# Kernel tuning notes

Hardware: AMD Instinct MI355X
Metric: run time of the kernel (lower is better)

## Reference

```python
import jax, jax.numpy as jnp
import numpy as np

NC = 80          # num classes (len(yolov8.names))
CONF = 0.25      # ultralytics conf_thres default
IOU_T = 0.45     # ultralytics iou_thres default
MAX_DET = 300    # module default max_det
K = 1024         # pre-NMS candidate cap (static stand-in for max_nms)
MAX_WH = 7680.0  # ultralytics class-offset for multi-class NMS


def setup_inputs() -> dict:
    key = jax.random.key(0)
    k1, k2, k3 = jax.random.split(key, 3)
    B, A = 32, 8400
    # YOLOv8 head layout: rows 0:4 = xywh (pixels), rows 4: = sigmoid class scores
    xy = jax.random.uniform(k1, (B, 2, A), dtype=jnp.float32) * 640.0
    wh = jax.random.uniform(k2, (B, 2, A), dtype=jnp.float32) * 160.0 + 8.0
    scores = jax.random.uniform(k3, (B, NC, A), dtype=jnp.float32) ** 3  # mostly below conf_thres
    preds = jnp.concatenate([xy, wh, scores], axis=1)  # [B, 4+NC, A]
    return {"preds": preds}


def _box_iou(b):
    # b: [K, 4] xyxy -> [K, K] pairwise IoU
    area = (b[:, 2] - b[:, 0]) * (b[:, 3] - b[:, 1])
    lt = jnp.maximum(b[:, None, :2], b[None, :, :2])
    rb = jnp.minimum(b[:, None, 2:], b[None, :, 2:])
    wh = jnp.clip(rb - lt, 0.0)
    inter = wh[..., 0] * wh[..., 1]
    return inter / (area[:, None] + area[None, :] - inter + 1e-7)


def _nms_single(pred):
    # pred: [4+NC, A]
    boxes_xywh = pred[:4].T           # [A, 4]
    cls_scores = pred[4:].T           # [A, NC]
    conf = cls_scores.max(-1)         # best-class confidence per anchor
    cls = jnp.argmax(cls_scores, -1)
    score = jnp.where(conf > CONF, conf, 0.0)
    top, idx = jax.lax.top_k(score, K)            # K candidates by confidence
    xywh = boxes_xywh[idx]
    half = xywh[:, 2:] * 0.5
    boxes = jnp.concatenate([xywh[:, :2] - half, xywh[:, :2] + half], -1)  # xyxy
    cls_k = cls[idx]
    valid = top > CONF
    # multi-class NMS via per-class coordinate offset (ultralytics trick)
    iou = _box_iou(boxes + (cls_k.astype(boxes.dtype) * MAX_WH)[:, None])
    ar = jnp.arange(K)

    def body(i, st):
        supp, keep = st
        ki = valid[i] & ~supp[i]
        keep = keep.at[i].set(ki)
        supp = supp | (ki & (iou[i] > IOU_T) & (ar > i))
        return supp, keep

    _, keep = jax.lax.fori_loop(0, K, body,
                                (jnp.zeros(K, bool), jnp.zeros(K, bool)))
    fscore = jnp.where(keep, top, 0.0)
    sc, order = jax.lax.top_k(fscore, MAX_DET)
    det = jnp.concatenate(
        [boxes[order], top[order][:, None], cls_k[order].astype(boxes.dtype)[:, None]], -1)
    # pad invalid rows with value NC in every column (matches F.pad(value=len(names)))
    return jnp.where((sc > CONF)[:, None], det, jnp.float32(NC))


def reference(preds):
    # [B, MAX_DET, 6] -> (x1, y1, x2, y2, conf, cls), padded rows filled with NC
    return jax.vmap(_nms_single)(preds)
```

## Files before the change

kernel.cpp:

```cpp
#include <hip/hip_runtime.h>
#include <stdint.h>

typedef unsigned long long u64;
typedef unsigned int u32;

#define NC 80
#define CONF_T 0.25f
#define IOU_THR 0.45f
#define MAX_DET 300
#define KBIG 1024
#define KSMALL 512
#define A_ANCH 8400
#define NROWS 84
#define MAX_WH 7680.0f

__global__ __launch_bounds__(256) void yolo_conf_kernel(const float* __restrict__ preds,
                                                        u64* __restrict__ keys) {
    int b = blockIdx.x / 9;
    int g = (blockIdx.x % 9) * 256 + threadIdx.x;
    if (g >= A_ANCH / 4) return;
    int a0 = g * 4;
    const float* base = preds + ((size_t)b * NROWS + 4) * A_ANCH + a0;
    float4 best = *(const float4*)base;
    int bcx = 0, bcy = 0, bcz = 0, bcw = 0;
#pragma unroll 4
    for (int c = 1; c < NC; ++c) {
        float4 v = *(const float4*)(base + (size_t)c * A_ANCH);
        if (v.x > best.x) { best.x = v.x; bcx = c; }
        if (v.y > best.y) { best.y = v.y; bcy = c; }
        if (v.z > best.z) { best.z = v.z; bcz = c; }
        if (v.w > best.w) { best.w = v.w; bcw = c; }
    }
    float s0 = (best.x > CONF_T) ? best.x : 0.0f;
    float s1 = (best.y > CONF_T) ? best.y : 0.0f;
    float s2 = (best.z > CONF_T) ? best.z : 0.0f;
    float s3 = (best.w > CONF_T) ? best.w : 0.0f;
    u64* ko = keys + (size_t)b * A_ANCH + a0;
    ulonglong2 k01, k23;
    k01.x = ((u64)__float_as_uint(s0) << 32) | ((u64)(16383 - a0) << 7) | (u64)bcx;
    k01.y = ((u64)__float_as_uint(s1) << 32) | ((u64)(16383 - (a0 + 1)) << 7) | (u64)bcy;
    k23.x = ((u64)__float_as_uint(s2) << 32) | ((u64)(16383 - (a0 + 2)) << 7) | (u64)bcz;
    k23.y = ((u64)__float_as_uint(s3) << 32) | ((u64)(16383 - (a0 + 3)) << 7) | (u64)bcw;
    *(ulonglong2*)ko = k01;
    *(ulonglong2*)(ko + 2) = k23;
}

__device__ __forceinline__ float iou_f(float ix1, float iy1, float ix2, float iy2, float iar,
                                       float jx1, float jy1, float jx2, float jy2, float jar) {
    float lx = fmaxf(ix1, jx1), ly = fmaxf(iy1, jy1);
    float rx = fminf(ix2, jx2), ry = fminf(iy2, jy2);
    float ww = fmaxf(__fsub_rn(rx, lx), 0.0f);
    float hh = fmaxf(__fsub_rn(ry, ly), 0.0f);
    float inter = __fmul_rn(ww, hh);
    float den = __fadd_rn(__fsub_rn(__fadd_rn(iar, jar), inter), 1e-7f);
    return __fdiv_rn(inter, den);
}

__device__ __forceinline__ void hadd(u32* h, u32 bin, bool m, int lane) {
    u64 act = __ballot(m);
    if (act == 0) return;
    int fl = __ffsll((unsigned long long)act) - 1;
    u32 fb = __shfl(bin, fl);
    u64 same = __ballot(m && (bin == fb));
    if (lane == fl) atomicAdd(&h[fb], (u32)__popcll(same));
    if (m && (bin != fb)) atomicAdd(&h[bin], 1u);
}

__device__ __forceinline__ u64 bstep(u64 v, u32 idx, u32 size, u32 stride) {
    u64 v2 = __shfl_xor((unsigned long long)v, (int)stride, 64);
    bool keep_big = (((idx & stride) == 0) == ((idx & size) == 0));
    return ((v > v2) == keep_big) ? v : v2;
}

__device__ __forceinline__ void radix_scan(u32* hist, int nb, int shift, u32* s_scal,
                                           u32* wsum, int tid, int lane, int wid) {
    int per = nb >> 10; if (per == 0) per = 1;
    int na = nb / per;
    u32 rem = s_scal[1];
    u32 Pk = s_scal[0];
    int hi = nb - 1 - per * tid;
    u32 s = 0;
    if (tid < na)
        for (int q = 0; q < per; ++q) s += hist[hi - q];
    u32 pre = s;
#pragma unroll
    for (int off = 1; off < 64; off <<= 1) {
        u32 o = __shfl_up(pre, off);
        if (lane >= off) pre += o;
    }
    if (lane == 63) wsum[wid] = pre;
    __syncthreads();
    u32 base = 0;
    for (int w = 0; w < wid; ++w) base += wsum[w];
    u32 run = base + pre - s;
    if (tid < na) {
        for (int q = 0; q < per; ++q) {
            int d = hi - q;
            u32 g = hist[d];
            if (run < rem && rem <= run + g) {
                s_scal[0] = Pk | ((u32)d << shift);
                s_scal[1] = rem - run;
            }
            run += g;
        }
    }
    __syncthreads();
}

union U2 {
    u32 hist[4096];
    struct { u32 eqw[264]; u32 wpre[264]; } tie;
};

__global__ __launch_bounds__(1024) void yolo_nms_kernel(const float* __restrict__ preds,
                                                        const u64* __restrict__ keys,
                                                        float* __restrict__ out) {
    const int b = blockIdx.x;
    const int tid = threadIdx.x;
    const int lane = tid & 63;
    const int wid = tid >> 6;

    __shared__ U2 u2;
    __shared__ u64 skey[KBIG];
    __shared__ float BX1[KBIG], BY1[KBIG], BX2[KBIG], BY2[KBIG], BAR[KBIG];
    __shared__ int keptlist[364];
    __shared__ float kx1[364], ky1[364], kx2[364], ky2[364], kar[364];
    __shared__ u32 kcls[364];
    __shared__ u64 rows[64];
    __shared__ u32 wsum[16];
    __shared__ u32 s_scal[4];
    __shared__ u32 s_csupp[2];
    __shared__ u32 s_nkept;
    __shared__ u32 s_valid;

    const u64* kb = keys + (size_t)b * A_ANCH;

    u32 vals[9];
#pragma unroll
    for (int it = 0; it < 9; ++it) {
        int a = tid + it * 1024;
        vals[it] = (a < A_ANCH) ? (u32)(kb[a] >> 32) : 0u;
    }

    for (int sel_pass = 0; sel_pass < 2; ++sel_pass) {
        const int K_sel = sel_pass ? KBIG : KSMALL;

        for (int i = tid; i < 4096; i += 1024) u2.hist[i] = 0;
        if (tid == 0) {
            s_scal[0] = 0; s_scal[1] = (u32)K_sel; s_scal[2] = 0;
            s_nkept = 0; s_csupp[0] = 0; s_csupp[1] = 0;
            if (sel_pass == 0) s_valid = 0;
        }
        __syncthreads();

#pragma unroll
        for (int it = 0; it < 9; ++it) {
            int a = tid + it * 1024;
            hadd(u2.hist, vals[it] >> 20, a < A_ANCH, lane);
        }
        if (sel_pass == 0) {
            u32 c = 0;
#pragma unroll
            for (int it = 0; it < 9; ++it) c += (vals[it] != 0u) ? 1u : 0u;
#pragma unroll
            for (int off = 32; off >= 1; off >>= 1) c += __shfl_xor(c, off);
            if (lane == 0) atomicAdd(&s_valid, c);
        }
        __syncthreads();
        radix_scan(u2.hist, 4096, 20, s_scal, wsum, tid, lane, wid);

        for (int i = tid; i < 4096; i += 1024) u2.hist[i] = 0;
        __syncthreads();
        u32 Pk = s_scal[0];
#pragma unroll
        for (int it = 0; it < 9; ++it) {
            int a = tid + it * 1024;
            u32 v = vals[it];
            bool m = (a < A_ANCH) && ((v & 0xFFF00000u) == Pk);
            hadd(u2.hist, (v >> 8) & 4095u, m, lane);
        }
        __syncthreads();
        radix_scan(u2.hist, 4096, 8, s_scal, wsum, tid, lane, wid);

        for (int i = tid; i < 256; i += 1024) u2.hist[i] = 0;
        __syncthreads();
        Pk = s_scal[0];
#pragma unroll
        for (int it = 0; it < 9; ++it) {
            int a = tid + it * 1024;
            u32 v = vals[it];
            bool m = (a < A_ANCH) && ((v & 0xFFFFFF00u) == Pk);
            hadd(u2.hist, v & 255u, m, lane);
        }
        __syncthreads();
        radix_scan(u2.hist, 256, 0, s_scal, wsum, tid, lane, wid);

        const u32 P = s_scal[0];
        const u32 tEq = s_scal[1];

        if (tid < 264) u2.tie.eqw[tid] = 0;
        __syncthreads();
#pragma unroll
        for (int it = 0; it < 9; ++it) {
            int a = tid + it * 1024;
            if (a < A_ANCH && vals[it] == P) atomicOr(&u2.tie.eqw[a >> 5], 1u << (a & 31));
        }
        __syncthreads();
        if (wid == 0) {
            u32 cw[5], loc = 0;
#pragma unroll
            for (int q = 0; q < 5; ++q) {
                int w2 = lane * 5 + q;
                u32 e = (w2 < 264) ? u2.tie.eqw[w2] : 0u;
                cw[q] = (u32)__popc(e); loc += cw[q];
            }
            u32 pre = loc;
#pragma unroll
            for (int off = 1; off < 64; off <<= 1) {
                u32 o = __shfl_up(pre, off);
                if (lane >= off) pre += o;
            }
            u32 run = pre - loc;
#pragma unroll
            for (int q = 0; q < 5; ++q) {
                int w2 = lane * 5 + q;
                if (w2 < 264) u2.tie.wpre[w2] = run;
                run += cw[q];
            }
        }
        __syncthreads();

#pragma unroll
        for (int it = 0; it < 9; ++it) {
            int a = tid + it * 1024;
            bool take = false;
            if (a < A_ANCH) {
                u32 v = vals[it];
                take = v > P;
                if (!take && v == P) {
                    u32 r = u2.tie.wpre[a >> 5] +
                            (u32)__popc(u2.tie.eqw[a >> 5] & ((1u << (a & 31)) - 1u));
                    take = (r < tEq);
                }
            }
            u64 m = __ballot(take);
            if (m) {
                int fl = __ffsll((unsigned long long)m) - 1;
                u32 basep = 0;
                if (lane == fl) basep = atomicAdd(&s_scal[2], (u32)__popcll(m));
                basep = __shfl(basep, fl);
                if (take) skey[basep + (u32)__popcll(m & ((1ull << lane) - 1ull))] = kb[a];
            }
        }
        __syncthreads();

        {
            const bool act = tid < K_sel;
            u64 v = act ? skey[tid] : 0;
            if (act) {
#pragma unroll
                for (u32 size = 2; size <= 64; size <<= 1)
#pragma unroll
                    for (u32 stride = size >> 1; stride >= 1; stride >>= 1)
                        v = bstep(v, (u32)tid, size, stride);
            }
            for (u32 size = 128; size <= (u32)K_sel; size <<= 1) {
                for (u32 stride = size >> 1; stride >= 64; stride >>= 1) {
                    if (act) skey[tid] = v;
                    __syncthreads();
                    if (act) {
                        u64 v2 = skey[tid ^ stride];
                        bool keep_big = ((((u32)tid & stride) == 0) == (((u32)tid & size) == 0));
                        v = ((v > v2) == keep_big) ? v : v2;
                    }
                    __syncthreads();
                }
                if (act) {
#pragma unroll
                    for (u32 stride = 32; stride >= 1; stride >>= 1)
                        v = bstep(v, (u32)tid, size, stride);
                }
            }
            if (act) skey[tid] = v;
            __syncthreads();
        }

        if (tid < K_sel) {
            u64 key = skey[tid];
            int cls = (int)(key & 127u);
            int idx = 16383 - (int)((key >> 7) & 16383u);
            const float* pb = preds + (size_t)b * NROWS * A_ANCH + idx;
            float x = pb[0];
            float y = pb[A_ANCH];
            float w = pb[2 * A_ANCH];
            float h = pb[3 * A_ANCH];
            float hw = __fmul_rn(w, 0.5f), hh = __fmul_rn(h, 0.5f);
            float x1 = __fsub_rn(x, hw), x2 = __fadd_rn(x, hw);
            float y1 = __fsub_rn(y, hh), y2 = __fadd_rn(y, hh);
            float off = __fmul_rn((float)cls, MAX_WH);
            float bx1 = __fadd_rn(x1, off), bx2 = __fadd_rn(x2, off);
            float by1 = __fadd_rn(y1, off), by2 = __fadd_rn(y2, off);
            BX1[tid] = bx1; BY1[tid] = by1; BX2[tid] = bx2; BY2[tid] = by2;
            BAR[tid] = __fmul_rn(__fsub_rn(bx2, bx1), __fsub_rn(by2, by1));
        }
        __syncthreads();

        const int nchunks = K_sel / 64;
        for (int c = 0; c < nchunks; ++c) {
            int j = c * 64 + lane;
            u64 keyj = skey[j];
            float scj = __uint_as_float((u32)(keyj >> 32));
            u32 clsj = (u32)(keyj & 127u);
            float jx1 = BX1[j], jy1 = BY1[j], jx2 = BX2[j], jy2 = BY2[j], jar = BAR[j];

            u32 nk = s_nkept;
            bool suppbit = false;
            for (u32 k = wid; k < nk; k += 16) {
                bool cm = (kcls[k] == clsj);
                if (__ballot(cm)) {
                    float iou = iou_f(kx1[k], ky1[k], kx2[k], ky2[k], kar[k],
                                      jx1, jy1, jx2, jy2, jar);
                    suppbit |= (cm && (iou > IOU_THR));
                }
            }
            u64 bm = __ballot(suppbit);
            if (bm && lane == 0) {
                atomicOr(&s_csupp[0], (u32)bm);
                atomicOr(&s_csupp[1], (u32)(bm >> 32));
            }

#pragma unroll
            for (int p2 = 0; p2 < 4; ++p2) {
                int i = p2 * 16 + wid;
                int ci = c * 64 + i;
                u32 clsi = (u32)(skey[ci] & 127u);
                u64 m = 0;
                if (__ballot(clsi == clsj)) {
                    float iou = iou_f(BX1[ci], BY1[ci], BX2[ci], BY2[ci], BAR[ci],
                                      jx1, jy1, jx2, jy2, jar);
                    m = __ballot((lane > i) && (iou > IOU_THR));
                }
                if (lane == 0) rows[i] = m;
            }
            __syncthreads();

            if (wid == 0) {
                u64 row = rows[lane];
                u32 rlo = (u32)row, rhi = (u32)(row >> 32);
                u64 csupp = (((u64)s_csupp[1]) << 32) | (u64)s_csupp[0];
                u64 validm = __ballot(scj > CONF_T) & ~csupp;
                u64 supp = 0, keep = 0;
#pragma unroll
                for (int i = 0; i < 64; ++i) {
                    u64 ri = (((u64)(u32)__builtin_amdgcn_readlane((int)rhi, i)) << 32) |
                             (u64)(u32)__builtin_amdgcn_readlane((int)rlo, i);
                    bool ki = (((validm & ~supp) >> i) & 1ull) != 0;
                    if (ki) { keep |= (1ull << i); supp |= ri; }
                }
                u32 basek = s_nkept;
                if ((keep >> lane) & 1ull) {
                    u32 slot = basek + (u32)__popcll(keep & ((1ull << lane) - 1ull));
                    keptlist[slot] = j;
                    kx1[slot] = jx1; ky1[slot] = jy1;
                    kx2[slot] = jx2; ky2[slot] = jy2;
                    kar[slot] = jar; kcls[slot] = clsj;
                }
                if (lane == 0) {
                    s_nkept = basek + (u32)__popcll(keep);
                    s_csupp[0] = 0; s_csupp[1] = 0;
                }
            }
            __syncthreads();
            if (s_nkept >= MAX_DET) break;
        }

        u32 nk = s_nkept;
        bool finished = (nk >= MAX_DET) || (s_valid <= (u32)K_sel) || (sel_pass == 1);
        if (!finished) { __syncthreads(); continue; }

        if (tid < MAX_DET) {
            float row[6];
            int t = (tid < (int)(nk < MAX_DET ? nk : MAX_DET)) ? keptlist[tid] : -1;
            if (t >= 0) {
                u64 key = skey[t];
                float score = __uint_as_float((u32)(key >> 32));
                int cls = (int)(key & 127u);
                int idx = 16383 - (int)((key >> 7) & 16383u);
                const float* pb = preds + (size_t)b * NROWS * A_ANCH + idx;
                float x = pb[0], y = pb[A_ANCH], w = pb[2 * A_ANCH], h = pb[3 * A_ANCH];
                float hw = __fmul_rn(w, 0.5f), hh = __fmul_rn(h, 0.5f);
                row[0] = __fsub_rn(x, hw);
                row[1] = __fsub_rn(y, hh);
                row[2] = __fadd_rn(x, hw);
                row[3] = __fadd_rn(y, hh);
                row[4] = score;
                row[5] = (float)cls;
            } else {
                row[0] = row[1] = row[2] = row[3] = row[4] = row[5] = (float)NC;
            }
            float* o = out + ((size_t)b * MAX_DET + tid) * 6;
#pragma unroll
            for (int q = 0; q < 6; ++q) o[q] = row[q];
        }
        break;
    }
}

extern "C" void kernel_launch(void* const* d_in, const int* in_sizes, int n_in,
                              void* d_out, int out_size, void* d_ws, size_t ws_size,
                              hipStream_t stream) {
    const float* preds = (const float*)d_in[0];
    float* out = (float*)d_out;
    u64* keys = (u64*)d_ws;
    int B = in_sizes[0] / (NROWS * A_ANCH);
    yolo_conf_kernel<<<dim3(B * 9), dim3(256), 0, stream>>>(preds, keys);
    yolo_nms_kernel<<<dim3(B), dim3(1024), 0, stream>>>(preds, keys, out);
}
```

Before: 73.77 us.

## Precompute boxes and global 16-bit score histogram in conf kernel for fast selection

The confidence kernel now also writes class-offset xyxy boxes and builds a per-image 65536-bin global histogram of the top 16 score bits using atomics. The NMS kernel scans that histogram to find a bin threshold that covers at least 512 candidates. It gathers all keys at or above that threshold (up to 1024) in one pass, skipping the three-level radix select, and sorts only those. It falls back to the full radix path when more than 1024 candidates qualify. The change adds a memset of the histogram, global atomics, and extra workspace writes in the first kernel.

```diff
diff --git a/kernel.cpp b/kernel.cpp
--- a/kernel.cpp
+++ b/kernel.cpp
@@ -9,13 +9,15 @@
 #define IOU_THR 0.45f
 #define MAX_DET 300
 #define KBIG 1024
-#define KSMALL 512
 #define A_ANCH 8400
 #define NROWS 84
 #define MAX_WH 7680.0f
+#define HBINS 65536
 
 __global__ __launch_bounds__(256) void yolo_conf_kernel(const float* __restrict__ preds,
-                                                        u64* __restrict__ keys) {
+                                                        u64* __restrict__ keys,
+                                                        float4* __restrict__ obox,
+                                                        u32* __restrict__ hist) {
     int b = blockIdx.x / 9;
     int g = (blockIdx.x % 9) * 256 + threadIdx.x;
     if (g >= A_ANCH / 4) return;
@@ -31,18 +33,40 @@
         if (v.z > best.z) { best.z = v.z; bcz = c; }
         if (v.w > best.w) { best.w = v.w; bcw = c; }
     }
-    float s0 = (best.x > CONF_T) ? best.x : 0.0f;
-    float s1 = (best.y > CONF_T) ? best.y : 0.0f;
-    float s2 = (best.z > CONF_T) ? best.z : 0.0f;
-    float s3 = (best.w > CONF_T) ? best.w : 0.0f;
+    float sc[4] = {(best.x > CONF_T) ? best.x : 0.0f, (best.y > CONF_T) ? best.y : 0.0f,
+                   (best.z > CONF_T) ? best.z : 0.0f, (best.w > CONF_T) ? best.w : 0.0f};
+    int cl[4] = {bcx, bcy, bcz, bcw};
     u64* ko = keys + (size_t)b * A_ANCH + a0;
     ulonglong2 k01, k23;
-    k01.x = ((u64)__float_as_uint(s0) << 32) | ((u64)(16383 - a0) << 7) | (u64)bcx;
-    k01.y = ((u64)__float_as_uint(s1) << 32) | ((u64)(16383 - (a0 + 1)) << 7) | (u64)bcy;
-    k23.x = ((u64)__float_as_uint(s2) << 32) | ((u64)(16383 - (a0 + 2)) << 7) | (u64)bcz;
-    k23.y = ((u64)__float_as_uint(s3) << 32) | ((u64)(16383 - (a0 + 3)) << 7) | (u64)bcw;
+    k01.x = ((u64)__float_as_uint(sc[0]) << 32) | ((u64)(16383 - a0) << 7) | (u64)cl[0];
+    k01.y = ((u64)__float_as_uint(sc[1]) << 32) | ((u64)(16383 - (a0 + 1)) << 7) | (u64)cl[1];
+    k23.x = ((u64)__float_as_uint(sc[2]) << 32) | ((u64)(16383 - (a0 + 2)) << 7) | (u64)cl[2];
+    k23.y = ((u64)__float_as_uint(sc[3]) << 32) | ((u64)(16383 - (a0 + 3)) << 7) | (u64)cl[3];
     *(ulonglong2*)ko = k01;
     *(ulonglong2*)(ko + 2) = k23;
+
+    const float* pb = preds + (size_t)b * NROWS * A_ANCH + a0;
+    float4 xv = *(const float4*)(pb);
+    float4 yv = *(const float4*)(pb + A_ANCH);
+    float4 wv = *(const float4*)(pb + 2 * A_ANCH);
+    float4 hv = *(const float4*)(pb + 3 * A_ANCH);
+    float xs[4] = {xv.x, xv.y, xv.z, xv.w};
+    float ys[4] = {yv.x, yv.y, yv.z, yv.w};
+    float ws[4] = {wv.x, wv.y, wv.z, wv.w};
+    float hs[4] = {hv.x, hv.y, hv.z, hv.w};
+    u32* hb = hist + (size_t)b * HBINS;
+#pragma unroll
+    for (int q = 0; q < 4; ++q) {
+        float hw = __fmul_rn(ws[q], 0.5f), hh = __fmul_rn(hs[q], 0.5f);
+        float x1 = __fsub_rn(xs[q], hw), x2 = __fadd_rn(xs[q], hw);
+        float y1 = __fsub_rn(ys[q], hh), y2 = __fadd_rn(ys[q], hh);
+        float off = __fmul_rn((float)cl[q], MAX_WH);
+        float4 ob;
+        ob.x = __fadd_rn(x1, off); ob.y = __fadd_rn(y1, off);
+        ob.z = __fadd_rn(x2, off); ob.w = __fadd_rn(y2, off);
+        obox[(size_t)b * A_ANCH + a0 + q] = ob;
+        atomicAdd(&hb[__float_as_uint(sc[q]) >> 16], 1u);
+    }
 }
 
 __device__ __forceinline__ float iou_f(float ix1, float iy1, float ix2, float iy2, float iar,
@@ -114,6 +138,8 @@
 
 __global__ __launch_bounds__(1024) void yolo_nms_kernel(const float* __restrict__ preds,
                                                         const u64* __restrict__ keys,
+                                                        const float4* __restrict__ obox,
+                                                        const u32* __restrict__ hist,
                                                         float* __restrict__ out) {
     const int b = blockIdx.x;
     const int tid = threadIdx.x;
@@ -141,171 +167,220 @@
         int a = tid + it * 1024;
         vals[it] = (a < A_ANCH) ? (u32)(kb[a] >> 32) : 0u;
     }
-
-    for (int sel_pass = 0; sel_pass < 2; ++sel_pass) {
-        const int K_sel = sel_pass ? KBIG : KSMALL;
-
-        for (int i = tid; i < 4096; i += 1024) u2.hist[i] = 0;
-        if (tid == 0) {
-            s_scal[0] = 0; s_scal[1] = (u32)K_sel; s_scal[2] = 0;
-            s_nkept = 0; s_csupp[0] = 0; s_csupp[1] = 0;
-            if (sel_pass == 0) s_valid = 0;
-        }
+    if (tid == 0) s_valid = 0;
+    __syncthreads();
+    {
+        u32 c = 0;
+#pragma unroll
+        for (int it = 0; it < 9; ++it) c += (vals[it] != 0u) ? 1u : 0u;
+#pragma unroll
+        for (int off = 32; off >= 1; off >>= 1) c += __shfl_xor(c, off);
+        if (lane == 0) atomicAdd(&s_valid, c);
+    }
+
+    const u32* hb = hist + (size_t)b * HBINS;
+    {
+        const uint4* hb4 = (const uint4*)hb;
+        u32 tsum = 0;
+#pragma unroll
+        for (int q = 0; q < 16; ++q) {
+            uint4 v = hb4[tid * 16 + q];
+            tsum += v.x + v.y + v.z + v.w;
+        }
+        u32 pre = tsum;
+#pragma unroll
+        for (int off = 1; off < 64; off <<= 1) {
+            u32 o = __shfl_down(pre, off);
+            if (lane + off < 64) pre += o;
+        }
+        if (lane == 0) wsum[wid] = pre;
         __syncthreads();
-
-#pragma unroll
-        for (int it = 0; it < 9; ++it) {
-            int a = tid + it * 1024;
-            hadd(u2.hist, vals[it] >> 20, a < A_ANCH, lane);
-        }
-        if (sel_pass == 0) {
-            u32 c = 0;
-#pragma unroll
-            for (int it = 0; it < 9; ++it) c += (vals[it] != 0u) ? 1u : 0u;
-#pragma unroll
-            for (int off = 32; off >= 1; off >>= 1) c += __shfl_xor(c, off);
-            if (lane == 0) atomicAdd(&s_valid, c);
-        }
-        __syncthreads();
-        radix_scan(u2.hist, 4096, 20, s_scal, wsum, tid, lane, wid);
-
-        for (int i = tid; i < 4096; i += 1024) u2.hist[i] = 0;
-        __syncthreads();
-        u32 Pk = s_scal[0];
-#pragma unroll
-        for (int it = 0; it < 9; ++it) {
-            int a = tid + it * 1024;
-            u32 v = vals[it];
-            bool m = (a < A_ANCH) && ((v & 0xFFF00000u) == Pk);
-            hadd(u2.hist, (v >> 8) & 4095u, m, lane);
-        }
-        __syncthreads();
-        radix_scan(u2.hist, 4096, 8, s_scal, wsum, tid, lane, wid);
-
-        for (int i = tid; i < 256; i += 1024) u2.hist[i] = 0;
-        __syncthreads();
-        Pk = s_scal[0];
-#pragma unroll
-        for (int it = 0; it < 9; ++it) {
-            int a = tid + it * 1024;
-            u32 v = vals[it];
-            bool m = (a < A_ANCH) && ((v & 0xFFFFFF00u) == Pk);
-            hadd(u2.hist, v & 255u, m, lane);
-        }
-        __syncthreads();
-        radix_scan(u2.hist, 256, 0, s_scal, wsum, tid, lane, wid);
-
-        const u32 P = s_scal[0];
-        const u32 tEq = s_scal[1];
-
-        if (tid < 264) u2.tie.eqw[tid] = 0;
-        __syncthreads();
-#pragma unroll
-        for (int it = 0; it < 9; ++it) {
-            int a = tid + it * 1024;
-            if (a < A_ANCH && vals[it] == P) atomicOr(&u2.tie.eqw[a >> 5], 1u << (a & 31));
-        }
+        u32 above = pre - tsum;
+        for (int w = wid + 1; w < 16; ++w) above += wsum[w];
+        if (above < 512u && 512u <= above + tsum) { s_scal[0] = (u32)tid; s_scal[1] = above; }
         __syncthreads();
         if (wid == 0) {
-            u32 cw[5], loc = 0;
-#pragma unroll
-            for (int q = 0; q < 5; ++q) {
-                int w2 = lane * 5 + q;
-                u32 e = (w2 < 264) ? u2.tie.eqw[w2] : 0u;
-                cw[q] = (u32)__popc(e); loc += cw[q];
-            }
-            u32 pre = loc;
+            u32 t = s_scal[0], baseAbove = s_scal[1];
+            u32 g = hb[t * 64 + 63 - lane];
+            u32 p = g;
 #pragma unroll
             for (int off = 1; off < 64; off <<= 1) {
-                u32 o = __shfl_up(pre, off);
-                if (lane >= off) pre += o;
-            }
-            u32 run = pre - loc;
-#pragma unroll
-            for (int q = 0; q < 5; ++q) {
-                int w2 = lane * 5 + q;
-                if (w2 < 264) u2.tie.wpre[w2] = run;
-                run += cw[q];
+                u32 o = __shfl_up(p, off);
+                if (lane >= off) p += o;
+            }
+            u32 run = baseAbove + p - g;
+            if (run < 512u && 512u <= run + g) {
+                s_scal[0] = t * 64 + 63 - lane;
+                s_scal[1] = run;
+                s_scal[2] = run + g;
             }
         }
         __syncthreads();
-
-#pragma unroll
-        for (int it = 0; it < 9; ++it) {
-            int a = tid + it * 1024;
-            bool take = false;
-            if (a < A_ANCH) {
+    }
+    const u32 Pbin = s_scal[0];
+    const u32 Cfast = s_scal[2];
+    const u32 validN = s_valid;
+
+    for (int pass = 0; pass < 2; ++pass) {
+        u32 Ccand;
+        if (pass == 0) {
+            if (Cfast > (u32)KBIG) continue;
+            Ccand = Cfast;
+            skey[tid] = 0;
+            if (tid == 0) { s_scal[3] = 0; s_nkept = 0; s_csupp[0] = 0; s_csupp[1] = 0; }
+            __syncthreads();
+#pragma unroll
+            for (int it = 0; it < 9; ++it) {
+                int a = tid + it * 1024;
+                bool take = (a < A_ANCH) && ((vals[it] >> 16) >= Pbin) && (vals[it] != 0u);
+                u64 m = __ballot(take);
+                if (m) {
+                    int fl = __ffsll((unsigned long long)m) - 1;
+                    u32 basep = 0;
+                    if (lane == fl) basep = atomicAdd(&s_scal[3], (u32)__popcll(m));
+                    basep = __shfl(basep, fl);
+                    if (take) {
+                        u32 pos = basep + (u32)__popcll(m & ((1ull << lane) - 1ull));
+                        if (pos < (u32)KBIG) skey[pos] = kb[a];
+                    }
+                }
+            }
+            __syncthreads();
+        } else {
+            for (int i = tid; i < 4096; i += 1024) u2.hist[i] = 0;
+            if (tid == 0) {
+                s_scal[0] = 0; s_scal[1] = (u32)KBIG; s_scal[2] = 0;
+                s_nkept = 0; s_csupp[0] = 0; s_csupp[1] = 0;
+            }
+            __syncthreads();
+#pragma unroll
+            for (int it = 0; it < 9; ++it) {
+                int a = tid + it * 1024;
+                hadd(u2.hist, vals[it] >> 20, a < A_ANCH, lane);
+            }
+            __syncthreads();
+            radix_scan(u2.hist, 4096, 20, s_scal, wsum, tid, lane, wid);
+            for (int i = tid; i < 4096; i += 1024) u2.hist[i] = 0;
+            __syncthreads();
+            u32 Pk = s_scal[0];
+#pragma unroll
+            for (int it = 0; it < 9; ++it) {
+                int a = tid + it * 1024;
                 u32 v = vals[it];
-                take = v > P;
-                if (!take && v == P) {
-                    u32 r = u2.tie.wpre[a >> 5] +
-                            (u32)__popc(u2.tie.eqw[a >> 5] & ((1u << (a & 31)) - 1u));
-                    take = (r < tEq);
-                }
-            }
-            u64 m = __ballot(take);
-            if (m) {
-                int fl = __ffsll((unsigned long long)m) - 1;
-                u32 basep = 0;
-                if (lane == fl) basep = atomicAdd(&s_scal[2], (u32)__popcll(m));
-                basep = __shfl(basep, fl);
-                if (take) skey[basep + (u32)__popcll(m & ((1ull << lane) - 1ull))] = kb[a];
-            }
+                bool m = (a < A_ANCH) && ((v & 0xFFF00000u) == Pk);
+                hadd(u2.hist, (v >> 8) & 4095u, m, lane);
+            }
+            __syncthreads();
+            radix_scan(u2.hist, 4096, 8, s_scal, wsum, tid, lane, wid);
+            for (int i = tid; i < 256; i += 1024) u2.hist[i] = 0;
+            __syncthreads();
+            Pk = s_scal[0];
+#pragma unroll
+            for (int it = 0; it < 9; ++it) {
+                int a = tid + it * 1024;
+                u32 v = vals[it];
+                bool m = (a < A_ANCH) && ((v & 0xFFFFFF00u) == Pk);
+                hadd(u2.hist, v & 255u, m, lane);
+            }
+            __syncthreads();
+            radix_scan(u2.hist, 256, 0, s_scal, wsum, tid, lane, wid);
+            const u32 P = s_scal[0];
+            const u32 tEq = s_scal[1];
+            if (tid < 264) u2.tie.eqw[tid] = 0;
+            __syncthreads();
+#pragma unroll
+            for (int it = 0; it < 9; ++it) {
+                int a = tid + it * 1024;
+                if (a < A_ANCH && vals[it] == P) atomicOr(&u2.tie.eqw[a >> 5], 1u << (a & 31));
+            }
+            __syncthreads();
+            if (wid == 0) {
+                u32 cw[5], loc = 0;
+#pragma unroll
+                for (int q = 0; q < 5; ++q) {
+                    int w2 = lane * 5 + q;
+                    u32 e = (w2 < 264) ? u2.tie.eqw[w2] : 0u;
+                    cw[q] = (u32)__popc(e); loc += cw[q];
+                }
+                u32 pre = loc;
+#pragma unroll
+                for (int off = 1; off < 64; off <<= 1) {
+                    u32 o = __shfl_up(pre, off);
+                    if (lane >= off) pre += o;
+                }
+                u32 run = pre - loc;
+#pragma unroll
+                for (int q = 0; q < 5; ++q) {
+                    int w2 = lane * 5 + q;
+                    if (w2 < 264) u2.tie.wpre[w2] = run;
+                    run += cw[q];
+                }
+            }
+            __syncthreads();
+#pragma unroll
+            for (int it = 0; it < 9; ++it) {
+                int a = tid + it * 1024;
+                bool take = false;
+                if (a < A_ANCH) {
+                    u32 v = vals[it];
+                    take = v > P;
+                    if (!take && v == P) {
+                        u32 r = u2.tie.wpre[a >> 5] +
+                                (u32)__popc(u2.tie.eqw[a >> 5] & ((1u << (a & 31)) - 1u));
+                        take = (r < tEq);
+                    }
+                }
+                u64 m = __ballot(take);
+                if (m) {
+                    int fl = __ffsll((unsigned long long)m) - 1;
+                    u32 basep = 0;
+                    if (lane == fl) basep = atomicAdd(&s_scal[2], (u32)__popcll(m));
+                    basep = __shfl(basep, fl);
+                    if (take) {
+                        u32 pos = basep + (u32)__popcll(m & ((1ull << lane) - 1ull));
+                        if (pos < (u32)KBIG) skey[pos] = kb[a];
+                    }
+                }
+            }
+            __syncthreads();
+            Ccand = KBIG;
+        }
+
+        {
+            u64 v = skey[tid];
+#pragma unroll
+            for (u32 size = 2; size <= 64; size <<= 1)
+#pragma unroll
+                for (u32 stride = size >> 1; stride >= 1; stride >>= 1)
+                    v = bstep(v, (u32)tid, size, stride);
+            for (u32 size = 128; size <= 1024; size <<= 1) {
+                for (u32 stride = size >> 1; stride >= 64; stride >>= 1) {
+                    skey[tid] = v;
+                    __syncthreads();
+                    u64 v2 = skey[tid ^ stride];
+                    bool keep_big = ((((u32)tid & stride) == 0) == (((u32)tid & size) == 0));
+                    v = ((v > v2) == keep_big) ? v : v2;
+                    __syncthreads();
+                }
+#pragma unroll
+                for (u32 stride = 32; stride >= 1; stride >>= 1)
+                    v = bstep(v, (u32)tid, size, stride);
+            }
+            skey[tid] = v;
+            __syncthreads();
+        }
+
+        {
+            u64 key = skey[tid];
+            int idx = 16383 - (int)((key >> 7) & 16383u);
+            if (idx >= A_ANCH || idx < 0) idx = 0;
+            float4 ob = obox[(size_t)b * A_ANCH + idx];
+            BX1[tid] = ob.x; BY1[tid] = ob.y; BX2[tid] = ob.z; BY2[tid] = ob.w;
+            BAR[tid] = __fmul_rn(__fsub_rn(ob.z, ob.x), __fsub_rn(ob.w, ob.y));
         }
         __syncthreads();
 
-        {
-            const bool act = tid < K_sel;
-            u64 v = act ? skey[tid] : 0;
-            if (act) {
-#pragma unroll
-                for (u32 size = 2; size <= 64; size <<= 1)
-#pragma unroll
-                    for (u32 stride = size >> 1; stride >= 1; stride >>= 1)
-                        v = bstep(v, (u32)tid, size, stride);
-            }
-            for (u32 size = 128; size <= (u32)K_sel; size <<= 1) {
-                for (u32 stride = size >> 1; stride >= 64; stride >>= 1) {
-                    if (act) skey[tid] = v;
-                    __syncthreads();
-                    if (act) {
-                        u64 v2 = skey[tid ^ stride];
-                        bool keep_big = ((((u32)tid & stride) == 0) == (((u32)tid & size) == 0));
-                        v = ((v > v2) == keep_big) ? v : v2;
-                    }
-                    __syncthreads();
-                }
-                if (act) {
-#pragma unroll
-                    for (u32 stride = 32; stride >= 1; stride >>= 1)
-                        v = bstep(v, (u32)tid, size, stride);
-                }
-            }
-            if (act) skey[tid] = v;
-            __syncthreads();
-        }
-
-        if (tid < K_sel) {
-            u64 key = skey[tid];
-            int cls = (int)(key & 127u);
-            int idx = 16383 - (int)((key >> 7) & 16383u);
-            const float* pb = preds + (size_t)b * NROWS * A_ANCH + idx;
-            float x = pb[0];
-            float y = pb[A_ANCH];
-            float w = pb[2 * A_ANCH];
-            float h = pb[3 * A_ANCH];
-            float hw = __fmul_rn(w, 0.5f), hh = __fmul_rn(h, 0.5f);
-            float x1 = __fsub_rn(x, hw), x2 = __fadd_rn(x, hw);
-            float y1 = __fsub_rn(y, hh), y2 = __fadd_rn(y, hh);
-            float off = __fmul_rn((float)cls, MAX_WH);
-            float bx1 = __fadd_rn(x1, off), bx2 = __fadd_rn(x2, off);
-            float by1 = __fadd_rn(y1, off), by2 = __fadd_rn(y2, off);
-            BX1[tid] = bx1; BY1[tid] = by1; BX2[tid] = bx2; BY2[tid] = by2;
-            BAR[tid] = __fmul_rn(__fsub_rn(bx2, bx1), __fsub_rn(by2, by1));
-        }
-        __syncthreads();
-
-        const int nchunks = K_sel / 64;
+        const int nchunks = (int)((Ccand + 63u) >> 6);
         for (int c = 0; c < nchunks; ++c) {
             int j = c * 64 + lane;
             u64 keyj = skey[j];
@@ -328,7 +403,6 @@
                 atomicOr(&s_csupp[0], (u32)bm);
                 atomicOr(&s_csupp[1], (u32)(bm >> 32));
             }
-
 #pragma unroll
             for (int p2 = 0; p2 < 4; ++p2) {
                 int i = p2 * 16 + wid;
@@ -343,7 +417,6 @@
                 if (lane == 0) rows[i] = m;
             }
             __syncthreads();
-
             if (wid == 0) {
                 u64 row = rows[lane];
                 u32 rlo = (u32)row, rhi = (u32)(row >> 32);
@@ -375,8 +448,8 @@
         }
 
         u32 nk = s_nkept;
-        bool finished = (nk >= MAX_DET) || (s_valid <= (u32)K_sel) || (sel_pass == 1);
-        if (!finished) { __syncthreads(); continue; }
+        bool finished = (nk >= MAX_DET) || (Ccand >= validN) || (pass == 1);
+        if (!finished) continue;
 
         if (tid < MAX_DET) {
             float row[6];
@@ -411,8 +484,11 @@
                               hipStream_t stream) {
     const float* preds = (const float*)d_in[0];
     float* out = (float*)d_out;
+    int B = in_sizes[0] / (NROWS * A_ANCH);
     u64* keys = (u64*)d_ws;
-    int B = in_sizes[0] / (NROWS * A_ANCH);
-    yolo_conf_kernel<<<dim3(B * 9), dim3(256), 0, stream>>>(preds, keys);
-    yolo_nms_kernel<<<dim3(B), dim3(1024), 0, stream>>>(preds, keys, out);
-}
+    float4* obox = (float4*)(keys + (size_t)B * A_ANCH);
+    u32* hist = (u32*)(obox + (size_t)B * A_ANCH);
+    (void)hipMemsetAsync(hist, 0, (size_t)B * HBINS * sizeof(u32), stream);
+    yolo_conf_kernel<<<dim3(B * 9), dim3(256), 0, stream>>>(preds, keys, obox, hist);
+    yolo_nms_kernel<<<dim3(B), dim3(1024), 0, stream>>>(preds, keys, obox, hist, out);
+}
```

After: 122.3 us. +65.8%, slower.
